# Kernel optimization log

Measured on AMD Instinct MI355X. Metric: run time of the kernel, lower is better.

## Reference

```python
import jax, jax.numpy as jnp
import numpy as np

B, S, H, DH = 2, 2048, 12, 64
D = H * DH          # dim_hidden = 768
DF = 4 * D          # dim_ffn = 3072
EPS = 1e-5


def layernorm(x, g, b):
    mu = jnp.mean(x, -1, keepdims=True)
    var = jnp.var(x, -1, keepdims=True)
    return (x - mu) * jax.lax.rsqrt(var + EPS) * g + b


def setup_inputs() -> dict:
    key = jax.random.key(0)
    ks = jax.random.split(key, 8)
    sc = 0.02
    x = jax.random.normal(ks[0], (B, S, D), jnp.float32)
    # causal mask: True where attention is NOT allowed (masked_fill semantics)
    causal = ~jnp.tril(jnp.ones((S, S), dtype=bool))
    attn_mask = jnp.broadcast_to(causal, (B, S, S))
    Wq = jax.random.normal(ks[1], (D, D), jnp.float32) * sc
    Wk = jax.random.normal(ks[2], (D, D), jnp.float32) * sc
    Wv = jax.random.normal(ks[3], (D, D), jnp.float32) * sc
    Wo = jax.random.normal(ks[4], (D, D), jnp.float32) * sc
    bo = jnp.zeros((D,), jnp.float32)
    g1 = jnp.ones((D,), jnp.float32)
    b1 = jnp.zeros((D,), jnp.float32)
    W1 = jax.random.normal(ks[5], (DF, D), jnp.float32) * sc  # conv1 (k=1) == linear
    bb1 = jnp.zeros((DF,), jnp.float32)
    W2 = jax.random.normal(ks[6], (D, DF), jnp.float32) * sc
    bb2 = jnp.zeros((D,), jnp.float32)
    g2 = jnp.ones((D,), jnp.float32)
    b2 = jnp.zeros((D,), jnp.float32)
    return dict(x=x, attn_mask=attn_mask, Wq=Wq, Wk=Wk, Wv=Wv, Wo=Wo, bo=bo,
                g1=g1, b1=b1, W1=W1, bb1=bb1, W2=W2, bb2=bb2, g2=g2, b2=b2)


def reference(x, attn_mask, Wq, Wk, Wv, Wo, bo, g1, b1, W1, bb1, W2, bb2, g2, b2):
    b, s, d = x.shape
    # projections and head split: (B, H, S, DH)
    q = (x @ Wq.T).reshape(b, s, H, DH).transpose(0, 2, 1, 3)
    k = (x @ Wk.T).reshape(b, s, H, DH).transpose(0, 2, 1, 3)
    v = (x @ Wv.T).reshape(b, s, H, DH).transpose(0, 2, 1, 3)
    scores = jnp.einsum('bhqd,bhkd->bhqk', q, k) / jnp.sqrt(jnp.float32(DH))
    scores = jnp.where(attn_mask[:, None, :, :], jnp.float32(-1e9), scores)
    attn_p = jax.nn.softmax(scores, axis=-1)          # (B, H, S, S)
    attn_v = jnp.einsum('bhqk,bhkd->bhqd', attn_p, v)
    attn_v = attn_v.transpose(0, 2, 1, 3).reshape(b, s, d)
    attn_out = attn_v @ Wo.T + bo
    h = layernorm(x + attn_out, g1, b1)
    f = jax.nn.gelu(h @ W1.T + bb1, approximate=False) @ W2.T + bb2
    y = layernorm(h + f, g2, b2)
    return y, attn_p
```

## Files before the change

### kernel.cpp

```cpp
#include <hip/hip_runtime.h>
#include <hip/hip_bf16.h>

#define DEV static __device__ __forceinline__

typedef short bf16x8  __attribute__((ext_vector_type(8)));
typedef short short4v __attribute__((ext_vector_type(4)));
typedef float f32x4   __attribute__((ext_vector_type(4)));

#define MFMA16(a,b,c) __builtin_amdgcn_mfma_f32_16x16x32_bf16((a),(b),(c),0,0,0)

DEV short f2b(float f) {
  unsigned u = __float_as_uint(f);
  unsigned r = (u + 0x7fffu + ((u >> 16) & 1u)) >> 16;
  return (short)r;
}

DEV void gld16(const void* g, void* l) {
  __builtin_amdgcn_global_load_lds(
      (const __attribute__((address_space(1))) unsigned int*)g,
      (__attribute__((address_space(3))) unsigned int*)l, 16, 0, 0);
}

DEV bf16x8 ldfrag(const short* tile, int row, int unit) {
  return *(const bf16x8*)(tile + row * 64 + (((unit) ^ (row & 7)) << 3));
}

__global__ __launch_bounds__(256) void cast4(const float4* __restrict__ in,
                                             short4v* __restrict__ out, int n4) {
  int i = blockIdx.x * 256 + threadIdx.x;
  if (i < n4) {
    float4 v = in[i];
    short4v o;
    o[0] = f2b(v.x); o[1] = f2b(v.y); o[2] = f2b(v.z); o[3] = f2b(v.w);
    out[i] = o;
  }
}

template <int MODE>
__global__ __launch_bounds__(256) void gemm_nt(
    const short* __restrict__ A, const short* __restrict__ Bw,
    float* __restrict__ outF, short* __restrict__ outB,
    short* __restrict__ outB2, short* __restrict__ outB3,
    const float* __restrict__ bias, const float* __restrict__ resid,
    int M, int N, int K, float scale) {
  __shared__ __align__(16) short As[128 * 32];
  __shared__ __align__(16) short Bs[128 * 32];
  int tid = threadIdx.x;
  int w = tid >> 6, lane = tid & 63, quad = lane >> 4, l15 = lane & 15;
  int m0 = blockIdx.x * 128, n0 = blockIdx.y * 128;
  int wm = (w & 1) * 64, wn = (w >> 1) * 64;
  f32x4 acc[4][4] = {};

  for (int k0 = 0; k0 < K; k0 += 32) {
    __syncthreads();
#pragma unroll
    for (int i = 0; i < 2; i++) {
      int id = i * 256 + tid;
      int r = id >> 2, c = id & 3;
      gld16(A + (size_t)(m0 + r) * K + k0 + c * 8, As + id * 8);
      gld16(Bw + (size_t)(n0 + r) * K + k0 + c * 8, Bs + id * 8);
    }
    __syncthreads();
    bf16x8 af[4], bfr[4];
#pragma unroll
    for (int mt = 0; mt < 4; mt++)
      af[mt] = *(const bf16x8*)(As + (wm + mt * 16 + l15) * 32 + quad * 8);
#pragma unroll
    for (int nt = 0; nt < 4; nt++)
      bfr[nt] = *(const bf16x8*)(Bs + (wn + nt * 16 + l15) * 32 + quad * 8);
#pragma unroll
    for (int mt = 0; mt < 4; mt++)
#pragma unroll
      for (int nt = 0; nt < 4; nt++)
        acc[mt][nt] = MFMA16(af[mt], bfr[nt], acc[mt][nt]);
  }

#pragma unroll
  for (int mt = 0; mt < 4; mt++) {
#pragma unroll
    for (int nt = 0; nt < 4; nt++) {
      if (MODE == 4 && n0 >= 1536) {
        int gcol = n0 + wn + nt * 16 + l15;
        int col = gcol - 1536;
        int h_ = col >> 6, d_ = col & 63;
        int srow = m0 + wm + mt * 16 + quad * 4;
        int b_ = srow >> 11, s_ = srow & 2047;
        short4v pk;
#pragma unroll
        for (int reg = 0; reg < 4; reg++) pk[reg] = f2b(acc[mt][nt][reg]);
        *(short4v*)(outB3 + ((size_t)(b_ * 12 + h_) * 64 + d_) * 2048 + s_) = pk;
      } else {
#pragma unroll
        for (int reg = 0; reg < 4; reg++) {
          int grow = m0 + wm + mt * 16 + quad * 4 + reg;
          int gcol = n0 + wn + nt * 16 + l15;
          float v = acc[mt][nt][reg];
          if (MODE == 2) {
            size_t idx = (size_t)grow * 768 + gcol;
            outF[idx] = v + bias[gcol] + resid[idx];
          } else if (MODE == 3) {
            float t = v + bias[gcol];
            float z = t * (1.0f + 0.044715f * t * t);
            float ge = t / (1.0f + __expf(-1.5957691216f * z));
            outB[(size_t)grow * N + gcol] = f2b(ge);
          } else if (MODE == 4) {
            int b_ = grow >> 11, s_ = grow & 2047;
            if (gcol < 768) {
              int h_ = gcol >> 6, d_ = gcol & 63;
              outB[(((size_t)(b_ * 12 + h_) << 11) + s_) * 64 + d_] = f2b(v * scale);
            } else {
              int col = gcol - 768;
              int h_ = col >> 6, d_ = col & 63;
              outB2[(((size_t)(b_ * 12 + h_) << 11) + s_) * 64 + d_] = f2b(v);
            }
          }
        }
      }
    }
  }
}

__global__ __launch_bounds__(256) void attn_kernel(
    const short* __restrict__ Qb, const short* __restrict__ Kb,
    const short* __restrict__ Vtb, float* __restrict__ Pout,
    short* __restrict__ Ov) {
  __shared__ __align__(16) short Qs[64 * 64];
  __shared__ __align__(16) short Ks[64 * 64];
  __shared__ __align__(16) short Vs[64 * 64];
  __shared__ __align__(16) short Ps[4 * 16 * 64];
  int tid = threadIdx.x, w = tid >> 6, lane = tid & 63;
  int quad = lane >> 4, l15 = lane & 15;
  int qb = (gridDim.x - 1) - blockIdx.x;
  int bh = blockIdx.y, q0 = qb << 6;
  const short* qp = Qb + ((size_t)bh << 17);
  const short* kp = Kb + ((size_t)bh << 17);
  const short* vp = Vtb + ((size_t)bh << 17);
  float* pp = Pout + ((size_t)bh << 22);

#pragma unroll
  for (int t = 0; t < 2; t++) {
    int row = t * 32 + w * 8 + (lane >> 3);
    int su = (lane & 7) ^ (row & 7);
    gld16(qp + ((size_t)(q0 + row) << 6) + su * 8, Qs + row * 64 + (lane & 7) * 8);
  }

  float lsum[4] = {0.f, 0.f, 0.f, 0.f};

  for (int kt = 0; kt <= qb; kt++) {
    __syncthreads();
#pragma unroll
    for (int t = 0; t < 2; t++) {
      int row = t * 32 + w * 8 + (lane >> 3);
      int su = (lane & 7) ^ (row & 7);
      gld16(kp + ((size_t)((kt << 6) + row) << 6) + su * 8,
            Ks + row * 64 + (lane & 7) * 8);
    }
    __syncthreads();
    f32x4 sc[4] = {};
    int arow = w * 16 + l15;
    bf16x8 a0 = ldfrag(Qs, arow, quad), a1 = ldfrag(Qs, arow, 4 + quad);
#pragma unroll
    for (int nt = 0; nt < 4; nt++) {
      int brow = nt * 16 + l15;
      bf16x8 b0 = ldfrag(Ks, brow, quad), b1 = ldfrag(Ks, brow, 4 + quad);
      sc[nt] = MFMA16(a0, b0, sc[nt]);
      sc[nt] = MFMA16(a1, b1, sc[nt]);
    }
    if (kt == qb) {
#pragma unroll
      for (int nt = 0; nt < 4; nt++) {
        int key = (kt << 6) + nt * 16 + l15;
#pragma unroll
        for (int reg = 0; reg < 4; reg++) {
          int qg = q0 + w * 16 + quad * 4 + reg;
          if (key > qg) sc[nt][reg] = -1e30f;
        }
      }
    }
#pragma unroll
    for (int reg = 0; reg < 4; reg++)
      lsum[reg] += __expf(sc[0][reg]) + __expf(sc[1][reg]) +
                   __expf(sc[2][reg]) + __expf(sc[3][reg]);
  }

  float rl[4];
#pragma unroll
  for (int reg = 0; reg < 4; reg++) {
    float s = lsum[reg];
#pragma unroll
    for (int xm = 1; xm < 16; xm <<= 1) s += __shfl_xor(s, xm, 64);
    rl[reg] = 1.0f / s;
  }
  f32x4 oacc[4] = {};

  for (int kt = 0; kt <= qb; kt++) {
    __syncthreads();
#pragma unroll
    for (int t = 0; t < 2; t++) {
      int row = t * 32 + w * 8 + (lane >> 3);
      int su = (lane & 7) ^ (row & 7);
      gld16(kp + ((size_t)((kt << 6) + row) << 6) + su * 8,
            Ks + row * 64 + (lane & 7) * 8);
      gld16(vp + (size_t)row * 2048 + (kt << 6) + su * 8,
            Vs + row * 64 + (lane & 7) * 8);
    }
    __syncthreads();
    f32x4 sc[4] = {};
    int arow = w * 16 + l15;
    bf16x8 a0 = ldfrag(Qs, arow, quad), a1 = ldfrag(Qs, arow, 4 + quad);
#pragma unroll
    for (int nt = 0; nt < 4; nt++) {
      int brow = nt * 16 + l15;
      bf16x8 b0 = ldfrag(Ks, brow, quad), b1 = ldfrag(Ks, brow, 4 + quad);
      sc[nt] = MFMA16(a0, b0, sc[nt]);
      sc[nt] = MFMA16(a1, b1, sc[nt]);
    }
    if (kt == qb) {
#pragma unroll
      for (int nt = 0; nt < 4; nt++) {
        int key = (kt << 6) + nt * 16 + l15;
#pragma unroll
        for (int reg = 0; reg < 4; reg++) {
          int qg = q0 + w * 16 + quad * 4 + reg;
          if (key > qg) sc[nt][reg] = -1e30f;
        }
      }
    }
#pragma unroll
    for (int nt = 0; nt < 4; nt++) {
      int key = (kt << 6) + nt * 16 + l15;
#pragma unroll
      for (int reg = 0; reg < 4; reg++) {
        int qg = q0 + w * 16 + quad * 4 + reg;
        float p = __expf(sc[nt][reg]) * rl[reg];
        pp[((size_t)qg << 11) + key] = p;
        int prow = quad * 4 + reg, pcol = nt * 16 + l15;
        Ps[(w << 10) + prow * 64 + (((pcol >> 3) ^ (prow & 7)) << 3) + (pcol & 7)] =
            f2b(p);
      }
    }
    bf16x8 p0 = ldfrag(Ps + (w << 10), l15, quad);
    bf16x8 p1 = ldfrag(Ps + (w << 10), l15, 4 + quad);
#pragma unroll
    for (int dn = 0; dn < 4; dn++) {
      int vrow = dn * 16 + l15;
      bf16x8 v0 = ldfrag(Vs, vrow, quad), v1 = ldfrag(Vs, vrow, 4 + quad);
      oacc[dn] = MFMA16(p0, v0, oacc[dn]);
      oacc[dn] = MFMA16(p1, v1, oacc[dn]);
    }
  }

  int b_ = bh / 12, h_ = bh - b_ * 12;
#pragma unroll
  for (int dn = 0; dn < 4; dn++)
#pragma unroll
    for (int reg = 0; reg < 4; reg++) {
      int s_ = q0 + w * 16 + quad * 4 + reg;
      Ov[(size_t)((b_ << 11) + s_) * 768 + h_ * 64 + dn * 16 + l15] =
          f2b(oacc[dn][reg]);
    }

  int kstart = (qb + 1) << 6;
  if (kstart < 2048) {
    int nch = (2048 - kstart) >> 2;
    for (int r = 0; r < 64; r++) {
      float4* dst = (float4*)(pp + ((size_t)(q0 + r) << 11) + kstart);
      for (int c = tid; c < nch; c += 256) dst[c] = make_float4(0.f, 0.f, 0.f, 0.f);
    }
  }
}

__global__ __launch_bounds__(256) void ln_kernel(
    const float* __restrict__ in, const float* __restrict__ gw,
    const float* __restrict__ bw, float* __restrict__ outF,
    short* __restrict__ outB) {
  int row = blockIdx.x, tid = threadIdx.x;
  const float* x = in + (size_t)row * 768;
  float v0 = x[tid], v1 = x[tid + 256], v2 = x[tid + 512];
  float s = v0 + v1 + v2;
  float ss = v0 * v0 + v1 * v1 + v2 * v2;
#pragma unroll
  for (int xm = 1; xm < 64; xm <<= 1) {
    s += __shfl_xor(s, xm, 64);
    ss += __shfl_xor(ss, xm, 64);
  }
  __shared__ float red[8];
  int w = tid >> 6, lane = tid & 63;
  if (lane == 0) { red[w] = s; red[w + 4] = ss; }
  __syncthreads();
  s = red[0] + red[1] + red[2] + red[3];
  ss = red[4] + red[5] + red[6] + red[7];
  float mu = s * (1.0f / 768.0f);
  float var = ss * (1.0f / 768.0f) - mu * mu;
  float inv = rsqrtf(var + 1e-5f);
  float* yF = outF + (size_t)row * 768;
#pragma unroll
  for (int i = 0; i < 3; i++) {
    int col = tid + i * 256;
    float v = (i == 0) ? v0 : (i == 1) ? v1 : v2;
    float y = (v - mu) * inv * gw[col] + bw[col];
    yF[col] = y;
    if (outB) outB[(size_t)row * 768 + col] = f2b(y);
  }
}

extern "C" void kernel_launch(void* const* d_in, const int* in_sizes, int n_in,
                              void* d_out, int out_size, void* d_ws, size_t ws_size,
                              hipStream_t stream) {
  const float* x  = (const float*)d_in[0];
  const float* Wq = (const float*)d_in[2];
  const float* Wk = (const float*)d_in[3];
  const float* Wv = (const float*)d_in[4];
  const float* Wo = (const float*)d_in[5];
  const float* bo = (const float*)d_in[6];
  const float* g1 = (const float*)d_in[7];
  const float* b1 = (const float*)d_in[8];
  const float* W1 = (const float*)d_in[9];
  const float* bb1 = (const float*)d_in[10];
  const float* W2 = (const float*)d_in[11];
  const float* bb2 = (const float*)d_in[12];
  const float* g2 = (const float*)d_in[13];
  const float* b2 = (const float*)d_in[14];

  char* cur = (char*)d_ws;
  auto take = [&](size_t n) { char* p = cur; cur += (n + 255) & ~(size_t)255; return p; };
  short* xb   = (short*)take((size_t)3145728 * 2);
  short* wqkv = (short*)take((size_t)2304 * 768 * 2);
  short* wob  = (short*)take((size_t)589824 * 2);
  short* w1b  = (short*)take((size_t)2359296 * 2);
  short* w2b  = (short*)take((size_t)2359296 * 2);
  short* qbf  = (short*)take((size_t)3145728 * 2);
  short* kbf  = (short*)take((size_t)3145728 * 2);
  short* vtb  = (short*)take((size_t)3145728 * 2);
  short* avb  = (short*)take((size_t)3145728 * 2);
  short* hb   = (short*)take((size_t)3145728 * 2);
  short* ub   = (short*)take((size_t)4096 * 3072 * 2);
  float* t1   = (float*)take((size_t)3145728 * 4);
  float* hf   = (float*)take((size_t)3145728 * 4);
  float* t2   = (float*)take((size_t)3145728 * 4);

  float* y_out = (float*)d_out;
  float* p_out = (float*)d_out + 3145728;

  cast4<<<3072, 256, 0, stream>>>((const float4*)x, (short4v*)xb, 786432);
  cast4<<<576, 256, 0, stream>>>((const float4*)Wq, (short4v*)(wqkv), 147456);
  cast4<<<576, 256, 0, stream>>>((const float4*)Wk, (short4v*)(wqkv + 589824), 147456);
  cast4<<<576, 256, 0, stream>>>((const float4*)Wv, (short4v*)(wqkv + 1179648), 147456);
  cast4<<<576, 256, 0, stream>>>((const float4*)Wo, (short4v*)wob, 147456);
  cast4<<<2304, 256, 0, stream>>>((const float4*)W1, (short4v*)w1b, 589824);
  cast4<<<2304, 256, 0, stream>>>((const float4*)W2, (short4v*)w2b, 589824);

  gemm_nt<4><<<dim3(32, 18), 256, 0, stream>>>(xb, wqkv, nullptr, qbf, kbf, vtb,
                                               nullptr, nullptr, 4096, 2304, 768, 0.125f);
  attn_kernel<<<dim3(32, 24), 256, 0, stream>>>(qbf, kbf, vtb, p_out, avb);
  gemm_nt<2><<<dim3(32, 6), 256, 0, stream>>>(avb, wob, t1, nullptr, nullptr, nullptr,
                                              bo, x, 4096, 768, 768, 1.0f);
  ln_kernel<<<4096, 256, 0, stream>>>(t1, g1, b1, hf, hb);
  gemm_nt<3><<<dim3(32, 24), 256, 0, stream>>>(hb, w1b, nullptr, ub, nullptr, nullptr,
                                               bb1, nullptr, 4096, 3072, 768, 1.0f);
  gemm_nt<2><<<dim3(32, 6), 256, 0, stream>>>(ub, w2b, t2, nullptr, nullptr, nullptr,
                                              bb2, hf, 4096, 768, 3072, 1.0f);
  ln_kernel<<<4096, 256, 0, stream>>>(t2, g2, b2, y_out, nullptr);
}
```

Measured before the change: 730.6 us.

## Load attention Q/K/V fragments directly from global memory and batch weight casts

The attention kernel drops its LDS staging of Q, K and V and the block-wide barriers around it. Each lane now reads its MFMA fragments straight from global memory into registers, and the MFMA sections run under raised wave priority. The six separate weight-cast launches are merged into two multi-tensor cast launches to cut launch overhead. In exchange, K and V data is no longer shared across the four waves through LDS, so redundant global or L2 reads rise, and the strided V loads may not coalesce well.

```diff
diff --git a/kernel.cpp b/kernel.cpp
--- a/kernel.cpp
+++ b/kernel.cpp
@@ -34,6 +34,22 @@
     o[0] = f2b(v.x); o[1] = f2b(v.y); o[2] = f2b(v.z); o[3] = f2b(v.w);
     out[i] = o;
   }
+}
+
+__global__ __launch_bounds__(256) void cast4_m(
+    const float4* __restrict__ s0, const float4* __restrict__ s1,
+    const float4* __restrict__ s2, const float4* __restrict__ s3,
+    short4v* __restrict__ d0, short4v* __restrict__ d1,
+    short4v* __restrict__ d2, short4v* __restrict__ d3, int n4) {
+  int i = blockIdx.x * 256 + threadIdx.x;
+  if (i >= n4) return;
+  int b = blockIdx.y;
+  const float4* s = (b == 0) ? s0 : (b == 1) ? s1 : (b == 2) ? s2 : s3;
+  short4v* d = (b == 0) ? d0 : (b == 1) ? d1 : (b == 2) ? d2 : d3;
+  float4 v = s[i];
+  short4v o;
+  o[0] = f2b(v.x); o[1] = f2b(v.y); o[2] = f2b(v.z); o[3] = f2b(v.w);
+  d[i] = o;
 }
 
 template <int MODE>
@@ -124,9 +140,6 @@
     const short* __restrict__ Qb, const short* __restrict__ Kb,
     const short* __restrict__ Vtb, float* __restrict__ Pout,
     short* __restrict__ Ov) {
-  __shared__ __align__(16) short Qs[64 * 64];
-  __shared__ __align__(16) short Ks[64 * 64];
-  __shared__ __align__(16) short Vs[64 * 64];
   __shared__ __align__(16) short Ps[4 * 16 * 64];
   int tid = threadIdx.x, w = tid >> 6, lane = tid & 63;
   int quad = lane >> 4, l15 = lane & 15;
@@ -137,35 +150,28 @@
   const short* vp = Vtb + ((size_t)bh << 17);
   float* pp = Pout + ((size_t)bh << 22);
 
-#pragma unroll
-  for (int t = 0; t < 2; t++) {
-    int row = t * 32 + w * 8 + (lane >> 3);
-    int su = (lane & 7) ^ (row & 7);
-    gld16(qp + ((size_t)(q0 + row) << 6) + su * 8, Qs + row * 64 + (lane & 7) * 8);
-  }
+  int arow = q0 + w * 16 + l15;
+  bf16x8 a0 = *(const bf16x8*)(qp + ((size_t)arow << 6) + quad * 8);
+  bf16x8 a1 = *(const bf16x8*)(qp + ((size_t)arow << 6) + 32 + quad * 8);
 
   float lsum[4] = {0.f, 0.f, 0.f, 0.f};
 
   for (int kt = 0; kt <= qb; kt++) {
-    __syncthreads();
-#pragma unroll
-    for (int t = 0; t < 2; t++) {
-      int row = t * 32 + w * 8 + (lane >> 3);
-      int su = (lane & 7) ^ (row & 7);
-      gld16(kp + ((size_t)((kt << 6) + row) << 6) + su * 8,
-            Ks + row * 64 + (lane & 7) * 8);
-    }
-    __syncthreads();
+    const short* kb = kp + ((size_t)kt << 12) + (size_t)l15 * 64 + quad * 8;
+    bf16x8 b[8];
+#pragma unroll
+    for (int nt = 0; nt < 4; nt++) {
+      b[2 * nt]     = *(const bf16x8*)(kb + nt * 1024);
+      b[2 * nt + 1] = *(const bf16x8*)(kb + nt * 1024 + 32);
+    }
     f32x4 sc[4] = {};
-    int arow = w * 16 + l15;
-    bf16x8 a0 = ldfrag(Qs, arow, quad), a1 = ldfrag(Qs, arow, 4 + quad);
-#pragma unroll
-    for (int nt = 0; nt < 4; nt++) {
-      int brow = nt * 16 + l15;
-      bf16x8 b0 = ldfrag(Ks, brow, quad), b1 = ldfrag(Ks, brow, 4 + quad);
-      sc[nt] = MFMA16(a0, b0, sc[nt]);
-      sc[nt] = MFMA16(a1, b1, sc[nt]);
-    }
+    __builtin_amdgcn_s_setprio(1);
+#pragma unroll
+    for (int nt = 0; nt < 4; nt++) {
+      sc[nt] = MFMA16(a0, b[2 * nt], sc[nt]);
+      sc[nt] = MFMA16(a1, b[2 * nt + 1], sc[nt]);
+    }
+    __builtin_amdgcn_s_setprio(0);
     if (kt == qb) {
 #pragma unroll
       for (int nt = 0; nt < 4; nt++) {
@@ -192,29 +198,24 @@
     rl[reg] = 1.0f / s;
   }
   f32x4 oacc[4] = {};
+  short* psw = Ps + (w << 10);
 
   for (int kt = 0; kt <= qb; kt++) {
-    __syncthreads();
-#pragma unroll
-    for (int t = 0; t < 2; t++) {
-      int row = t * 32 + w * 8 + (lane >> 3);
-      int su = (lane & 7) ^ (row & 7);
-      gld16(kp + ((size_t)((kt << 6) + row) << 6) + su * 8,
-            Ks + row * 64 + (lane & 7) * 8);
-      gld16(vp + (size_t)row * 2048 + (kt << 6) + su * 8,
-            Vs + row * 64 + (lane & 7) * 8);
-    }
-    __syncthreads();
+    const short* kb = kp + ((size_t)kt << 12) + (size_t)l15 * 64 + quad * 8;
+    bf16x8 b[8];
+#pragma unroll
+    for (int nt = 0; nt < 4; nt++) {
+      b[2 * nt]     = *(const bf16x8*)(kb + nt * 1024);
+      b[2 * nt + 1] = *(const bf16x8*)(kb + nt * 1024 + 32);
+    }
     f32x4 sc[4] = {};
-    int arow = w * 16 + l15;
-    bf16x8 a0 = ldfrag(Qs, arow, quad), a1 = ldfrag(Qs, arow, 4 + quad);
-#pragma unroll
-    for (int nt = 0; nt < 4; nt++) {
-      int brow = nt * 16 + l15;
-      bf16x8 b0 = ldfrag(Ks, brow, quad), b1 = ldfrag(Ks, brow, 4 + quad);
-      sc[nt] = MFMA16(a0, b0, sc[nt]);
-      sc[nt] = MFMA16(a1, b1, sc[nt]);
-    }
+    __builtin_amdgcn_s_setprio(1);
+#pragma unroll
+    for (int nt = 0; nt < 4; nt++) {
+      sc[nt] = MFMA16(a0, b[2 * nt], sc[nt]);
+      sc[nt] = MFMA16(a1, b[2 * nt + 1], sc[nt]);
+    }
+    __builtin_amdgcn_s_setprio(0);
     if (kt == qb) {
 #pragma unroll
       for (int nt = 0; nt < 4; nt++) {
@@ -235,19 +236,25 @@
         float p = __expf(sc[nt][reg]) * rl[reg];
         pp[((size_t)qg << 11) + key] = p;
         int prow = quad * 4 + reg, pcol = nt * 16 + l15;
-        Ps[(w << 10) + prow * 64 + (((pcol >> 3) ^ (prow & 7)) << 3) + (pcol & 7)] =
-            f2b(p);
+        psw[prow * 64 + (((pcol >> 3) ^ (prow & 7)) << 3) + (pcol & 7)] = f2b(p);
       }
     }
-    bf16x8 p0 = ldfrag(Ps + (w << 10), l15, quad);
-    bf16x8 p1 = ldfrag(Ps + (w << 10), l15, 4 + quad);
+    bf16x8 p0 = ldfrag(psw, l15, quad);
+    bf16x8 p1 = ldfrag(psw, l15, 4 + quad);
+    const short* vb = vp + ((size_t)l15 << 11) + (kt << 6) + quad * 8;
+    bf16x8 vf[8];
 #pragma unroll
     for (int dn = 0; dn < 4; dn++) {
-      int vrow = dn * 16 + l15;
-      bf16x8 v0 = ldfrag(Vs, vrow, quad), v1 = ldfrag(Vs, vrow, 4 + quad);
-      oacc[dn] = MFMA16(p0, v0, oacc[dn]);
-      oacc[dn] = MFMA16(p1, v1, oacc[dn]);
-    }
+      vf[2 * dn]     = *(const bf16x8*)(vb + dn * 32768);
+      vf[2 * dn + 1] = *(const bf16x8*)(vb + dn * 32768 + 32);
+    }
+    __builtin_amdgcn_s_setprio(1);
+#pragma unroll
+    for (int dn = 0; dn < 4; dn++) {
+      oacc[dn] = MFMA16(p0, vf[2 * dn], oacc[dn]);
+      oacc[dn] = MFMA16(p1, vf[2 * dn + 1], oacc[dn]);
+    }
+    __builtin_amdgcn_s_setprio(0);
   }
 
   int b_ = bh / 12, h_ = bh - b_ * 12;
@@ -343,12 +350,13 @@
   float* p_out = (float*)d_out + 3145728;
 
   cast4<<<3072, 256, 0, stream>>>((const float4*)x, (short4v*)xb, 786432);
-  cast4<<<576, 256, 0, stream>>>((const float4*)Wq, (short4v*)(wqkv), 147456);
-  cast4<<<576, 256, 0, stream>>>((const float4*)Wk, (short4v*)(wqkv + 589824), 147456);
-  cast4<<<576, 256, 0, stream>>>((const float4*)Wv, (short4v*)(wqkv + 1179648), 147456);
-  cast4<<<576, 256, 0, stream>>>((const float4*)Wo, (short4v*)wob, 147456);
-  cast4<<<2304, 256, 0, stream>>>((const float4*)W1, (short4v*)w1b, 589824);
-  cast4<<<2304, 256, 0, stream>>>((const float4*)W2, (short4v*)w2b, 589824);
+  cast4_m<<<dim3(576, 4), 256, 0, stream>>>(
+      (const float4*)Wq, (const float4*)Wk, (const float4*)Wv, (const float4*)Wo,
+      (short4v*)wqkv, (short4v*)(wqkv + 589824), (short4v*)(wqkv + 1179648),
+      (short4v*)wob, 147456);
+  cast4_m<<<dim3(2304, 2), 256, 0, stream>>>(
+      (const float4*)W1, (const float4*)W2, (const float4*)W1, (const float4*)W2,
+      (short4v*)w1b, (short4v*)w2b, (short4v*)w1b, (short4v*)w2b, 589824);
 
   gemm_nt<4><<<dim3(32, 18), 256, 0, stream>>>(xb, wqkv, nullptr, qbf, kbf, vtb,
                                                nullptr, nullptr, 4096, 2304, 768, 0.125f);
```

Result: slower. 874.2 us (+19.7%).

## Split-K the N=768 GEMMs, widen K tile to 64 with swizzle, fuse reduction into layernorm

Applied to the files above, without the earlier changes.

The two GEMMs with N=768 (only 192 blocks) are split along K into 2 and 4 slices written as fp32 partials. The partials are summed, together with bias and residual, inside the layernorm kernel. The GEMM K-tile grows from 32 to 64 with XOR-swizzled LDS layout to cut barriers and bank conflicts, and weight casts are merged into fewer launches. The split adds extra fp32 partial traffic in exchange for better CU occupancy.

```diff
diff --git a/kernel.cpp b/kernel.cpp
--- a/kernel.cpp
+++ b/kernel.cpp
@@ -36,44 +36,69 @@
   }
 }
 
+__global__ __launch_bounds__(256) void cast4_m(
+    const float4* __restrict__ s0, const float4* __restrict__ s1,
+    const float4* __restrict__ s2, const float4* __restrict__ s3,
+    short4v* __restrict__ d0, short4v* __restrict__ d1,
+    short4v* __restrict__ d2, short4v* __restrict__ d3, int n4) {
+  int i = blockIdx.x * 256 + threadIdx.x;
+  if (i >= n4) return;
+  int b = blockIdx.y;
+  const float4* s = (b == 0) ? s0 : (b == 1) ? s1 : (b == 2) ? s2 : s3;
+  short4v* d = (b == 0) ? d0 : (b == 1) ? d1 : (b == 2) ? d2 : d3;
+  float4 v = s[i];
+  short4v o;
+  o[0] = f2b(v.x); o[1] = f2b(v.y); o[2] = f2b(v.z); o[3] = f2b(v.w);
+  d[i] = o;
+}
+
 template <int MODE>
 __global__ __launch_bounds__(256) void gemm_nt(
     const short* __restrict__ A, const short* __restrict__ Bw,
     float* __restrict__ outF, short* __restrict__ outB,
     short* __restrict__ outB2, short* __restrict__ outB3,
-    const float* __restrict__ bias, const float* __restrict__ resid,
-    int M, int N, int K, float scale) {
-  __shared__ __align__(16) short As[128 * 32];
-  __shared__ __align__(16) short Bs[128 * 32];
+    const float* __restrict__ bias, int M, int N, int K, int Kstride,
+    float scale) {
+  __shared__ __align__(16) short As[128 * 64];
+  __shared__ __align__(16) short Bs[128 * 64];
   int tid = threadIdx.x;
   int w = tid >> 6, lane = tid & 63, quad = lane >> 4, l15 = lane & 15;
   int m0 = blockIdx.x * 128, n0 = blockIdx.y * 128;
+  int kbase = blockIdx.z * K;
+  const short* Ap = A + kbase;
+  const short* Bp = Bw + kbase;
   int wm = (w & 1) * 64, wn = (w >> 1) * 64;
   f32x4 acc[4][4] = {};
 
-  for (int k0 = 0; k0 < K; k0 += 32) {
-    __syncthreads();
-#pragma unroll
-    for (int i = 0; i < 2; i++) {
+  for (int k0 = 0; k0 < K; k0 += 64) {
+    __syncthreads();
+#pragma unroll
+    for (int i = 0; i < 4; i++) {
       int id = i * 256 + tid;
-      int r = id >> 2, c = id & 3;
-      gld16(A + (size_t)(m0 + r) * K + k0 + c * 8, As + id * 8);
-      gld16(Bw + (size_t)(n0 + r) * K + k0 + c * 8, Bs + id * 8);
-    }
-    __syncthreads();
-    bf16x8 af[4], bfr[4];
-#pragma unroll
-    for (int mt = 0; mt < 4; mt++)
-      af[mt] = *(const bf16x8*)(As + (wm + mt * 16 + l15) * 32 + quad * 8);
-#pragma unroll
-    for (int nt = 0; nt < 4; nt++)
-      bfr[nt] = *(const bf16x8*)(Bs + (wn + nt * 16 + l15) * 32 + quad * 8);
-#pragma unroll
-    for (int mt = 0; mt < 4; mt++)
+      int r = id >> 3, u = id & 7;
+      int su = u ^ (r & 7);
+      gld16(Ap + (size_t)(m0 + r) * Kstride + k0 + su * 8, As + id * 8);
+      gld16(Bp + (size_t)(n0 + r) * Kstride + k0 + su * 8, Bs + id * 8);
+    }
+    __syncthreads();
+#pragma unroll
+    for (int kk = 0; kk < 2; kk++) {
+      bf16x8 af[4], bfr[4];
+#pragma unroll
+      for (int mt = 0; mt < 4; mt++)
+        af[mt] = ldfrag(As, wm + mt * 16 + l15, kk * 4 + quad);
 #pragma unroll
       for (int nt = 0; nt < 4; nt++)
-        acc[mt][nt] = MFMA16(af[mt], bfr[nt], acc[mt][nt]);
-  }
+        bfr[nt] = ldfrag(Bs, wn + nt * 16 + l15, kk * 4 + quad);
+#pragma unroll
+      for (int mt = 0; mt < 4; mt++)
+#pragma unroll
+        for (int nt = 0; nt < 4; nt++)
+          acc[mt][nt] = MFMA16(af[mt], bfr[nt], acc[mt][nt]);
+    }
+  }
+
+  if (MODE == 0) outF += (size_t)blockIdx.z * M * N;
 
 #pragma unroll
   for (int mt = 0; mt < 4; mt++) {
@@ -95,9 +120,8 @@
           int grow = m0 + wm + mt * 16 + quad * 4 + reg;
           int gcol = n0 + wn + nt * 16 + l15;
           float v = acc[mt][nt][reg];
-          if (MODE == 2) {
-            size_t idx = (size_t)grow * 768 + gcol;
-            outF[idx] = v + bias[gcol] + resid[idx];
+          if (MODE == 0) {
+            outF[(size_t)grow * N + gcol] = v;
           } else if (MODE == 3) {
             float t = v + bias[gcol];
             float z = t * (1.0f + 0.044715f * t * t);
@@ -270,15 +294,27 @@
   }
 }
 
-__global__ __launch_bounds__(256) void ln_kernel(
-    const float* __restrict__ in, const float* __restrict__ gw,
-    const float* __restrict__ bw, float* __restrict__ outF,
-    short* __restrict__ outB) {
+template <int NP>
+__global__ __launch_bounds__(256) void ln_fuse(
+    const float* __restrict__ p0, const float* __restrict__ p1,
+    const float* __restrict__ p2, const float* __restrict__ p3,
+    const float* __restrict__ resid, const float* __restrict__ bias,
+    const float* __restrict__ gw, const float* __restrict__ bw,
+    float* __restrict__ outF, short* __restrict__ outB) {
   int row = blockIdx.x, tid = threadIdx.x;
-  const float* x = in + (size_t)row * 768;
-  float v0 = x[tid], v1 = x[tid + 256], v2 = x[tid + 512];
-  float s = v0 + v1 + v2;
-  float ss = v0 * v0 + v1 * v1 + v2 * v2;
+  size_t off = (size_t)row * 768;
+  float v[3];
+#pragma unroll
+  for (int i = 0; i < 3; i++) {
+    int col = tid + i * 256;
+    float t = p0[off + col] + resid[off + col] + bias[col];
+    if (NP > 1) t += p1[off + col];
+    if (NP > 2) t += p2[off + col];
+    if (NP > 3) t += p3[off + col];
+    v[i] = t;
+  }
+  float s = v[0] + v[1] + v[2];
+  float ss = v[0] * v[0] + v[1] * v[1] + v[2] * v[2];
 #pragma unroll
   for (int xm = 1; xm < 64; xm <<= 1) {
     s += __shfl_xor(s, xm, 64);
@@ -293,14 +329,13 @@
   float mu = s * (1.0f / 768.0f);
   float var = ss * (1.0f / 768.0f) - mu * mu;
   float inv = rsqrtf(var + 1e-5f);
-  float* yF = outF + (size_t)row * 768;
+  float* yF = outF + off;
 #pragma unroll
   for (int i = 0; i < 3; i++) {
     int col = tid + i * 256;
-    float v = (i == 0) ? v0 : (i == 1) ? v1 : v2;
-    float y = (v - mu) * inv * gw[col] + bw[col];
+    float y = (v[i] - mu) * inv * gw[col] + bw[col];
     yF[col] = y;
-    if (outB) outB[(size_t)row * 768 + col] = f2b(y);
+    if (outB) outB[off + col] = f2b(y);
   }
 }
 
@@ -322,43 +357,48 @@
   const float* g2 = (const float*)d_in[13];
   const float* b2 = (const float*)d_in[14];
 
+  const size_t P = (size_t)4096 * 768;
+
   char* cur = (char*)d_ws;
   auto take = [&](size_t n) { char* p = cur; cur += (n + 255) & ~(size_t)255; return p; };
-  short* xb   = (short*)take((size_t)3145728 * 2);
+  short* xb   = (short*)take(P * 2);
   short* wqkv = (short*)take((size_t)2304 * 768 * 2);
   short* wob  = (short*)take((size_t)589824 * 2);
   short* w1b  = (short*)take((size_t)2359296 * 2);
   short* w2b  = (short*)take((size_t)2359296 * 2);
-  short* qbf  = (short*)take((size_t)3145728 * 2);
-  short* kbf  = (short*)take((size_t)3145728 * 2);
-  short* vtb  = (short*)take((size_t)3145728 * 2);
-  short* avb  = (short*)take((size_t)3145728 * 2);
-  short* hb   = (short*)take((size_t)3145728 * 2);
+  short* qbf  = (short*)take(P * 2);
+  short* kbf  = (short*)take(P * 2);
+  short* vtb  = (short*)take(P * 2);
+  short* avb  = (short*)take(P * 2);
+  short* hb   = (short*)take(P * 2);
   short* ub   = (short*)take((size_t)4096 * 3072 * 2);
-  float* t1   = (float*)take((size_t)3145728 * 4);
-  float* hf   = (float*)take((size_t)3145728 * 4);
-  float* t2   = (float*)take((size_t)3145728 * 4);
+  float* t1   = (float*)take(P * 2 * 4);
+  float* hf   = (float*)take(P * 4);
+  float* t2   = (float*)take(P * 4 * 4);
 
   float* y_out = (float*)d_out;
-  float* p_out = (float*)d_out + 3145728;
+  float* p_out = (float*)d_out + P;
 
   cast4<<<3072, 256, 0, stream>>>((const float4*)x, (short4v*)xb, 786432);
-  cast4<<<576, 256, 0, stream>>>((const float4*)Wq, (short4v*)(wqkv), 147456);
-  cast4<<<576, 256, 0, stream>>>((const float4*)Wk, (short4v*)(wqkv + 589824), 147456);
-  cast4<<<576, 256, 0, stream>>>((const float4*)Wv, (short4v*)(wqkv + 1179648), 147456);
-  cast4<<<576, 256, 0, stream>>>((const float4*)Wo, (short4v*)wob, 147456);
-  cast4<<<2304, 256, 0, stream>>>((const float4*)W1, (short4v*)w1b, 589824);
-  cast4<<<2304, 256, 0, stream>>>((const float4*)W2, (short4v*)w2b, 589824);
-
-  gemm_nt<4><<<dim3(32, 18), 256, 0, stream>>>(xb, wqkv, nullptr, qbf, kbf, vtb,
-                                               nullptr, nullptr, 4096, 2304, 768, 0.125f);
+  cast4_m<<<dim3(576, 4), 256, 0, stream>>>(
+      (const float4*)Wq, (const float4*)Wk, (const float4*)Wv, (const float4*)Wo,
+      (short4v*)wqkv, (short4v*)(wqkv + 589824), (short4v*)(wqkv + 1179648),
+      (short4v*)wob, 147456);
+  cast4_m<<<dim3(2304, 2), 256, 0, stream>>>(
+      (const float4*)W1, (const float4*)W2, (const float4*)W1, (const float4*)W2,
+      (short4v*)w1b, (short4v*)w2b, (short4v*)w1b, (short4v*)w2b, 589824);
+
+  gemm_nt<4><<<dim3(32, 18), 256, 0, stream>>>(
+      xb, wqkv, nullptr, qbf, kbf, vtb, nullptr, 4096, 2304, 768, 768, 0.125f);
   attn_kernel<<<dim3(32, 24), 256, 0, stream>>>(qbf, kbf, vtb, p_out, avb);
-  gemm_nt<2><<<dim3(32, 6), 256, 0, stream>>>(avb, wob, t1, nullptr, nullptr, nullptr,
-                                              bo, x, 4096, 768, 768, 1.0f);
-  ln_kernel<<<4096, 256, 0, stream>>>(t1, g1, b1, hf, hb);
-  gemm_nt<3><<<dim3(32, 24), 256, 0, stream>>>(hb, w1b, nullptr, ub, nullptr, nullptr,
-                                               bb1, nullptr, 4096, 3072, 768, 1.0f);
-  gemm_nt<2><<<dim3(32, 6), 256, 0, stream>>>(ub, w2b, t2, nullptr, nullptr, nullptr,
-                                              bb2, hf, 4096, 768, 3072, 1.0f);
-  ln_kernel<<<4096, 256, 0, stream>>>(t2, g2, b2, y_out, nullptr);
-}
+  gemm_nt<0><<<dim3(32, 6, 2), 256, 0, stream>>>(
+      avb, wob, t1, nullptr, nullptr, nullptr, nullptr, 4096, 768, 384, 768, 1.0f);
+  ln_fuse<2><<<4096, 256, 0, stream>>>(t1, t1 + P, nullptr, nullptr, x, bo,
+                                       g1, b1, hf, hb);
+  gemm_nt<3><<<dim3(32, 24), 256, 0, stream>>>(
+      hb, w1b, nullptr, ub, nullptr, nullptr, bb1, 4096, 3072, 768, 768, 1.0f);
+  gemm_nt<0><<<dim3(32, 6, 4), 256, 0, stream>>>(
+      ub, w2b, t2, nullptr, nullptr, nullptr, nullptr, 4096, 768, 768, 3072, 1.0f);
+  ln_fuse<4><<<4096, 256, 0, stream>>>(t2, t2 + P, t2 + 2 * P, t2 + 3 * P, hf, bb2,
+                                       g2, b2, y_out, nullptr);
+}
```

After: 699.3 us. -4.3%, faster.
